# Performance work log

Hardware: AMD Instinct MI355X
Metric: run time of the kernel (lower is better)

The kernel has to match this reference:

```python
import jax, jax.numpy as jnp
import numpy as np

B, C, H, W = 16, 1024, 32, 32  # H*W must equal C (required by matmul(h, fg) in the source)
EPS = 1e-5
NEG_SLOPE = 0.01


def setup_inputs() -> dict:
    key = jax.random.key(0)
    ks = jax.random.split(key, 12)
    s = 1.0 / np.sqrt(C)
    inp = {"x": jax.random.normal(ks[0], (B, C, H, W), jnp.float32)}
    for i, name in enumerate(["f", "g", "h", "c"]):
        inp[f"W{name}"] = jax.random.normal(ks[1 + 2 * i], (C, C), jnp.float32) * s
        inp[f"b{name}"] = jax.random.normal(ks[2 + 2 * i], (C,), jnp.float32) * 0.01
    inp["gamma"] = jnp.ones((C,), jnp.float32)
    inp["beta"] = jnp.zeros((C,), jnp.float32)
    inp["rmean"] = jax.random.normal(ks[9], (C,), jnp.float32) * 0.01
    inp["rvar"] = jax.random.uniform(ks[10], (C,), jnp.float32, 0.5, 1.5)
    return inp


def reference(x, Wf, bf, Wg, bg, Wh, bh, Wc, bc, gamma, beta, rmean, rvar):
    b, c, h_, w_ = x.shape
    n = h_ * w_  # == c by construction
    xf = x.reshape(b, c, n)

    def proj(Wp, bp):  # 1x1 conv == per-pixel channel matmul
        return jnp.einsum('oc,bcn->bon', Wp, xf) + bp[None, :, None]

    f = proj(Wf, bf)              # (B, C, N)
    g = proj(Wg, bg)              # (B, C, N); transposed(1,2) handled in einsum
    hh = proj(Wh, bh)             # (B, C, N)
    scores = jnp.einsum('bcn,bdn->bcd', f, g)        # f @ g^T -> (B, C, C)
    attn = jax.nn.softmax(scores, axis=1)            # softmax over dim=1 (as in source)
    # dropout2d(p=0.5) is identity in eval mode
    hfg = jnp.einsum('bcn,bnd->bcd', hh, attn)       # matmul(h, fg), needs N == C
    hfg = hfg.reshape(b, c, h_, w_)
    y = jnp.einsum('oc,bchw->bohw', Wc, hfg) + bc[None, :, None, None]
    y = jnp.where(y >= 0, y, NEG_SLOPE * y)          # LeakyReLU
    inv = gamma / jnp.sqrt(rvar + EPS)               # BatchNorm (eval mode)
    y = (y - rmean[None, :, None, None]) * inv[None, :, None, None] + beta[None, :, None, None]
    return y + x
```

## Files before the change

kernel.cpp:

```cpp
#include <hip/hip_runtime.h>
#include <cstdint>
#include <cstddef>

using half8  = __attribute__((ext_vector_type(8))) _Float16;
using half4  = __attribute__((ext_vector_type(4))) _Float16;
using float4v = __attribute__((ext_vector_type(4))) float;

#define CD 1024
#define M2 (1024 * 1024)

#define GLD16(gp, lp)                                                          \
    __builtin_amdgcn_global_load_lds(                                          \
        (const __attribute__((address_space(1))) void*)(gp),                   \
        (__attribute__((address_space(3))) void*)(lp), 16, 0, 0)

__global__ void prep_weights(const float* __restrict__ Wf, const float* __restrict__ Wg,
                             const float* __restrict__ Wh, const float* __restrict__ Wc,
                             const float* __restrict__ bf, const float* __restrict__ bg,
                             const float* __restrict__ bh,
                             _Float16* __restrict__ Wfgh, _Float16* __restrict__ WcH,
                             float* __restrict__ bstack) {
    int idx = blockIdx.x * 256 + threadIdx.x;
    if (idx < 3 * M2) {
        const float* s = idx < M2 ? Wf : (idx < 2 * M2 ? Wg : Wh);
        int off = idx & (M2 - 1);
        Wfgh[idx] = (_Float16)s[off];
    } else if (idx < 4 * M2) {
        WcH[idx - 3 * M2] = (_Float16)Wc[idx - 3 * M2];
    } else if (idx < 4 * M2 + 3 * CD) {
        int j = idx - 4 * M2;
        const float* s = j < CD ? bf : (j < 2 * CD ? bg : bh);
        bstack[j] = s[j & (CD - 1)];
    }
}

__global__ void transpose_x(const float* __restrict__ x, _Float16* __restrict__ xT, int b0) {
    __shared__ float tile[32][33];
    int z = blockIdx.z;
    const float* xb = x + (size_t)(b0 + z) * M2;
    _Float16* xTb = xT + (size_t)z * M2;
    int n0 = blockIdx.x * 32, k0 = blockIdx.y * 32;
    int tx = threadIdx.x, ty = threadIdx.y;
#pragma unroll
    for (int i = 0; i < 4; i++)
        tile[ty + i * 8][tx] = xb[(size_t)(k0 + ty + i * 8) * CD + n0 + tx];
    __syncthreads();
#pragma unroll
    for (int i = 0; i < 4; i++)
        xTb[(size_t)(n0 + ty + i * 8) * CD + k0 + tx] = (_Float16)tile[tx][ty + i * 8];
}

__global__ __launch_bounds__(256) void softmax_col(const float* __restrict__ ST,
                                                   _Float16* __restrict__ attnT) {
    int d = blockIdx.x, z = blockIdx.y;
    const float* row = ST + ((size_t)z * CD + d) * CD;
    _Float16* orow = attnT + ((size_t)z * CD + d) * CD;
    int t = threadIdx.x;
    float4v v = *(const float4v*)(row + t * 4);
    float mx = fmaxf(fmaxf(v[0], v[1]), fmaxf(v[2], v[3]));
#pragma unroll
    for (int o = 32; o > 0; o >>= 1) mx = fmaxf(mx, __shfl_xor(mx, o));
    __shared__ float redm[4], reds[4];
    int wave = t >> 6, lane = t & 63;
    if (lane == 0) redm[wave] = mx;
    __syncthreads();
    mx = fmaxf(fmaxf(redm[0], redm[1]), fmaxf(redm[2], redm[3]));
    float e[4];
    float s = 0.f;
#pragma unroll
    for (int i = 0; i < 4; i++) {
        e[i] = __expf(v[i] - mx);
        s += e[i];
    }
#pragma unroll
    for (int o = 32; o > 0; o >>= 1) s += __shfl_xor(s, o);
    if (lane == 0) reds[wave] = s;
    __syncthreads();
    s = reds[0] + reds[1] + reds[2] + reds[3];
    float inv = 1.0f / s;
    half4 ov;
#pragma unroll
    for (int i = 0; i < 4; i++) ov[i] = (_Float16)(e[i] * inv);
    *(half4*)(orow + t * 4) = ov;
}

enum { EP_F16B = 0, EP_F32 = 1, EP_F16 = 2, EP_FIN = 3 };

#define STAGE_A(T, BUF)                                                        \
    GLD16(gA0 + (size_t)(T) * 32, &As[BUF][wv * 16][0]);                       \
    GLD16(gA1 + (size_t)(T) * 32, &As[BUF][128 + wv * 16][0]);
#define STAGE_B(T, BUF)                                                        \
    GLD16(gB0 + (size_t)(T) * 32, &Bs[BUF][wv * 16][0]);                       \
    GLD16(gB1 + (size_t)(T) * 32, &Bs[BUF][128 + wv * 16][0]);

#define MFMA_HALF(M0)                                                          \
    __builtin_amdgcn_s_setprio(1);                                             \
    _Pragma("unroll") for (int m = M0; m < (M0) + 4; m++)                      \
        _Pragma("unroll") for (int n = 0; n < 4; n++)                          \
            acc[m][n] = __builtin_amdgcn_mfma_f32_16x16x32_f16(                \
                a[m], b[n], acc[m][n], 0, 0, 0);                               \
    __builtin_amdgcn_s_setprio(0);

#define PHASE_A(BUF, SA, SAT, SAB)                                             \
    {                                                                          \
        _Pragma("unroll") for (int m = 0; m < 4; m++)                          \
            a[m] = *(const half8*)&As[BUF][wr * 128 + m * 16 + rl][kqa];       \
        _Pragma("unroll") for (int n = 0; n < 4; n++)                          \
            b[n] = *(const half8*)&Bs[BUF][wc * 64 + n * 16 + rl][kqa];        \
        if (SA) { STAGE_A(SAT, SAB) }                                          \
        __builtin_amdgcn_s_barrier();                                          \
        asm volatile("s_waitcnt lgkmcnt(0)" ::: "memory");                     \
        __builtin_amdgcn_sched_barrier(0);                                     \
        MFMA_HALF(0)                                                           \
        __builtin_amdgcn_s_barrier();                                          \
    }

#define PHASE_B(BUF, SB, SBT, SBB, VM, VMS, EBAR)                              \
    {                                                                          \
        _Pragma("unroll") for (int m = 4; m < 8; m++)                          \
            a[m] = *(const half8*)&As[BUF][wr * 128 + m * 16 + rl][kqa];       \
        if (SB) { STAGE_B(SBT, SBB) }                                          \
        __builtin_amdgcn_s_barrier();                                          \
        asm volatile("s_waitcnt lgkmcnt(0)" ::: "memory");                     \
        __builtin_amdgcn_sched_barrier(0);                                     \
        MFMA_HALF(4)                                                           \
        if (VM) {                                                              \
            asm volatile("s_waitcnt " VMS ::: "memory");                       \
            __builtin_amdgcn_sched_barrier(0);                                 \
        }                                                                      \
        if (EBAR) __builtin_amdgcn_s_barrier();                                \
    }

template <int EPI>
__global__ __launch_bounds__(512, 2) void gemm_nt(
    const _Float16* __restrict__ A, int64_t sA, const _Float16* __restrict__ B, int64_t sB,
    void* __restrict__ Cp, int64_t sC, const float* __restrict__ bias,
    const float* __restrict__ bc, const float* __restrict__ gamma,
    const float* __restrict__ beta, const float* __restrict__ rmean,
    const float* __restrict__ rvar, const float* __restrict__ xres) {
    __shared__ __align__(16) _Float16 As[4][256][32];
    __shared__ __align__(16) _Float16 Bs[4][256][32];
    int z = blockIdx.z;
    const _Float16* Ab = A + (size_t)z * sA;
    const _Float16* Bb = B + (size_t)z * sB;
    int row0 = blockIdx.y * 256, col0 = blockIdx.x * 256;
    int tid = threadIdx.x, lane = tid & 63, wv = tid >> 6;
    int wr = wv >> 2, wc = wv & 3;

    const int srow = wv * 16 + (lane >> 2);
    const int scol = ((lane & 3) ^ ((lane >> 3) & 3)) * 8;
    const _Float16* gA0 = Ab + (size_t)(row0 + srow) * 1024 + scol;
    const _Float16* gA1 = gA0 + (size_t)128 * 1024;
    const _Float16* gB0 = Bb + (size_t)(col0 + srow) * 1024 + scol;
    const _Float16* gB1 = gB0 + (size_t)128 * 1024;

    const int rl = lane & 15;
    const int kq = (lane >> 4) * 8;
    const int kqa = kq ^ (((rl >> 1) & 3) << 3);

    float4v acc[8][4] = {};
    half8 a[8], b[4];

    STAGE_A(0, 0) STAGE_B(0, 0) STAGE_A(1, 1) STAGE_B(1, 1)
    STAGE_A(2, 2) STAGE_B(2, 2) STAGE_B(3, 3)
    asm volatile("s_waitcnt vmcnt(10)" ::: "memory");
    __builtin_amdgcn_sched_barrier(0);
    __builtin_amdgcn_s_barrier();

#pragma unroll 1
    for (int tq = 0; tq < 7; ++tq) {
        int t = tq * 4;
        PHASE_A(0, 1, t + 3, 3) PHASE_B(0, 1, t + 4, 0, 1, "vmcnt(10)", 1)
        PHASE_A(1, 1, t + 4, 0) PHASE_B(1, 1, t + 5, 1, 1, "vmcnt(10)", 1)
        PHASE_A(2, 1, t + 5, 1) PHASE_B(2, 1, t + 6, 2, 1, "vmcnt(10)", 1)
        PHASE_A(3, 1, t + 6, 2) PHASE_B(3, 1, t + 7, 3, 1, "vmcnt(10)", 1)
    }
    PHASE_A(0, 1, 31, 3) PHASE_B(0, 0, 0, 0, 1, "vmcnt(8)", 1)
    PHASE_A(1, 0, 0, 0)  PHASE_B(1, 0, 0, 0, 1, "vmcnt(4)", 1)
    PHASE_A(2, 0, 0, 0)  PHASE_B(2, 0, 0, 0, 1, "vmcnt(0)", 1)
    PHASE_A(3, 0, 0, 0)  PHASE_B(3, 0, 0, 0, 0, "", 0)

#pragma unroll
    for (int m = 0; m < 8; m++) {
#pragma unroll
        for (int r = 0; r < 4; r++) {
            int row = row0 + wr * 128 + m * 16 + ((lane >> 4) << 2) + r;
            float add0 = 0.f, mu = 0.f, invs = 1.f, bet = 0.f;
            if constexpr (EPI == EP_F16B) add0 = bias[row];
            if constexpr (EPI == EP_FIN) {
                add0 = bc[row];
                mu = rmean[row];
                invs = gamma[row] * rsqrtf(rvar[row] + 1e-5f);
                bet = beta[row];
            }
#pragma unroll
            for (int n = 0; n < 4; n++) {
                int col = col0 + wc * 64 + n * 16 + (lane & 15);
                float v = acc[m][n][r];
                if constexpr (EPI == EP_F16B) {
                    ((_Float16*)Cp)[(size_t)z * sC + (size_t)row * 1024 + col] = (_Float16)(v + add0);
                } else if constexpr (EPI == EP_F32) {
                    ((float*)Cp)[(size_t)z * sC + (size_t)row * 1024 + col] = v;
                } else if constexpr (EPI == EP_F16) {
                    ((_Float16*)Cp)[(size_t)z * sC + (size_t)row * 1024 + col] = (_Float16)v;
                } else {
                    v += add0;
                    v = v >= 0.f ? v : 0.01f * v;
                    v = (v - mu) * invs + bet;
                    v += xres[(size_t)z * M2 + (size_t)row * 1024 + col];
                    ((float*)Cp)[(size_t)z * sC + (size_t)row * 1024 + col] = v;
                }
            }
        }
    }
}

extern "C" void kernel_launch(void* const* d_in, const int* in_sizes, int n_in,
                              void* d_out, int out_size, void* d_ws, size_t ws_size,
                              hipStream_t stream) {
    const float* x = (const float*)d_in[0];
    const float* Wf = (const float*)d_in[1];
    const float* bf = (const float*)d_in[2];
    const float* Wg = (const float*)d_in[3];
    const float* bg = (const float*)d_in[4];
    const float* Wh = (const float*)d_in[5];
    const float* bh = (const float*)d_in[6];
    const float* Wc = (const float*)d_in[7];
    const float* bc = (const float*)d_in[8];
    const float* gamma = (const float*)d_in[9];
    const float* beta = (const float*)d_in[10];
    const float* rmean = (const float*)d_in[11];
    const float* rvar = (const float*)d_in[12];

    char* p = (char*)d_ws;
    _Float16* Wfgh = (_Float16*)p;
    p += (size_t)3 * M2 * 2;
    _Float16* WcH = (_Float16*)p;
    p += (size_t)M2 * 2;
    float* bstack = (float*)p;
    p += (size_t)3 * CD * 4;
    size_t fixed = (size_t)(p - (char*)d_ws);
    fixed = (fixed + 255) & ~(size_t)255;

    size_t perB = (size_t)2 * M2 + (size_t)6 * M2 + (size_t)4 * M2;
    int nb = 16;
    while (nb > 1 && fixed + (size_t)nb * perB > ws_size) nb >>= 1;

    {
        int total = 4 * M2 + 3 * CD;
        prep_weights<<<dim3((total + 255) / 256), dim3(256), 0, stream>>>(
            Wf, Wg, Wh, Wc, bf, bg, bh, Wfgh, WcH, bstack);
    }

    for (int b0 = 0; b0 < 16; b0 += nb) {
        char* q = (char*)d_ws + fixed;
        _Float16* xT = (_Float16*)q;
        _Float16* FGH = (_Float16*)(q + (size_t)nb * 2 * M2);
        float* ST = (float*)(q + (size_t)nb * 8 * M2);
        _Float16* attnT = xT;
        _Float16* hfgT = (_Float16*)ST;

        transpose_x<<<dim3(32, 32, nb), dim3(32, 8), 0, stream>>>(x, xT, b0);
        gemm_nt<EP_F16B><<<dim3(4, 12, nb), dim3(512), 0, stream>>>(
            Wfgh, 0, xT, M2, FGH, (int64_t)3 * M2, bstack,
            nullptr, nullptr, nullptr, nullptr, nullptr, nullptr);
        gemm_nt<EP_F32><<<dim3(4, 4, nb), dim3(512), 0, stream>>>(
            FGH + M2, (int64_t)3 * M2, FGH, (int64_t)3 * M2, ST, M2,
            nullptr, nullptr, nullptr, nullptr, nullptr, nullptr, nullptr);
        softmax_col<<<dim3(1024, nb), dim3(256), 0, stream>>>(ST, attnT);
        gemm_nt<EP_F16><<<dim3(4, 4, nb), dim3(512), 0, stream>>>(
            attnT, M2, FGH + 2 * M2, (int64_t)3 * M2, hfgT, M2,
            nullptr, nullptr, nullptr, nullptr, nullptr, nullptr, nullptr);
        gemm_nt<EP_FIN><<<dim3(4, 4, nb), dim3(512), 0, stream>>>(
            WcH, 0, hfgT, M2, (float*)d_out + (size_t)b0 * M2, M2,
            nullptr, bc, gamma, beta, rmean, rvar, x + (size_t)b0 * M2);
    }
}
```

Measured before the change: 311.8 us.

## Collapse two-phase half-tile GEMM schedule into one barrier per K-tile

Replaces the split PHASE_A/PHASE_B main loop with a single TILE step per K-tile. Each step waits on global loads, takes one workgroup barrier, reads all A/B fragments from LDS, issues the A and B prefetch together, then runs all 32 MFMAs at raised priority. The prologue now stages three full tiles and the vmcnt thresholds are adjusted to match. This cuts the barriers per tile from four to one, but gives up the finer interleaving of LDS reads and global prefetch with the two MFMA halves.

```diff
diff --git a/kernel.cpp b/kernel.cpp
--- a/kernel.cpp
+++ b/kernel.cpp
@@ -93,42 +93,25 @@
     GLD16(gB0 + (size_t)(T) * 32, &Bs[BUF][wv * 16][0]);                       \
     GLD16(gB1 + (size_t)(T) * 32, &Bs[BUF][128 + wv * 16][0]);
 
-#define MFMA_HALF(M0)                                                          \
-    __builtin_amdgcn_s_setprio(1);                                             \
-    _Pragma("unroll") for (int m = M0; m < (M0) + 4; m++)                      \
-        _Pragma("unroll") for (int n = 0; n < 4; n++)                          \
-            acc[m][n] = __builtin_amdgcn_mfma_f32_16x16x32_f16(                \
-                a[m], b[n], acc[m][n], 0, 0, 0);                               \
-    __builtin_amdgcn_s_setprio(0);
-
-#define PHASE_A(BUF, SA, SAT, SAB)                                             \
+#define TILE(BUF, DOSTAGE, STT, STBUF, VMSTR)                                  \
     {                                                                          \
+        asm volatile("s_waitcnt " VMSTR ::: "memory");                         \
+        __builtin_amdgcn_sched_barrier(0);                                     \
+        __builtin_amdgcn_s_barrier();                                          \
         _Pragma("unroll") for (int m = 0; m < 4; m++)                          \
             a[m] = *(const half8*)&As[BUF][wr * 128 + m * 16 + rl][kqa];       \
         _Pragma("unroll") for (int n = 0; n < 4; n++)                          \
             b[n] = *(const half8*)&Bs[BUF][wc * 64 + n * 16 + rl][kqa];        \
-        if (SA) { STAGE_A(SAT, SAB) }                                          \
-        __builtin_amdgcn_s_barrier();                                          \
-        asm volatile("s_waitcnt lgkmcnt(0)" ::: "memory");                     \
-        __builtin_amdgcn_sched_barrier(0);                                     \
-        MFMA_HALF(0)                                                           \
-        __builtin_amdgcn_s_barrier();                                          \
-    }
-
-#define PHASE_B(BUF, SB, SBT, SBB, VM, VMS, EBAR)                              \
-    {                                                                          \
         _Pragma("unroll") for (int m = 4; m < 8; m++)                          \
             a[m] = *(const half8*)&As[BUF][wr * 128 + m * 16 + rl][kqa];       \
-        if (SB) { STAGE_B(SBT, SBB) }                                          \
-        __builtin_amdgcn_s_barrier();                                          \
-        asm volatile("s_waitcnt lgkmcnt(0)" ::: "memory");                     \
+        if (DOSTAGE) { STAGE_A(STT, STBUF) STAGE_B(STT, STBUF) }               \
         __builtin_amdgcn_sched_barrier(0);                                     \
-        MFMA_HALF(4)                                                           \
-        if (VM) {                                                              \
-            asm volatile("s_waitcnt " VMS ::: "memory");                       \
-            __builtin_amdgcn_sched_barrier(0);                                 \
-        }                                                                      \
-        if (EBAR) __builtin_amdgcn_s_barrier();                                \
+        __builtin_amdgcn_s_setprio(1);                                         \
+        _Pragma("unroll") for (int m = 0; m < 8; m++)                          \
+            _Pragma("unroll") for (int n = 0; n < 4; n++)                      \
+                acc[m][n] = __builtin_amdgcn_mfma_f32_16x16x32_f16(            \
+                    a[m], b[n], acc[m][n], 0, 0, 0);                           \
+        __builtin_amdgcn_s_setprio(0);                                         \
     }
 
 template <int EPI>
@@ -161,24 +144,22 @@
     float4v acc[8][4] = {};
     half8 a[8], b[4];
 
-    STAGE_A(0, 0) STAGE_B(0, 0) STAGE_A(1, 1) STAGE_B(1, 1)
-    STAGE_A(2, 2) STAGE_B(2, 2) STAGE_B(3, 3)
-    asm volatile("s_waitcnt vmcnt(10)" ::: "memory");
-    __builtin_amdgcn_sched_barrier(0);
-    __builtin_amdgcn_s_barrier();
+    STAGE_A(0, 0) STAGE_B(0, 0)
+    STAGE_A(1, 1) STAGE_B(1, 1)
+    STAGE_A(2, 2) STAGE_B(2, 2)
 
 #pragma unroll 1
-    for (int tq = 0; tq < 7; ++tq) {
-        int t = tq * 4;
-        PHASE_A(0, 1, t + 3, 3) PHASE_B(0, 1, t + 4, 0, 1, "vmcnt(10)", 1)
-        PHASE_A(1, 1, t + 4, 0) PHASE_B(1, 1, t + 5, 1, 1, "vmcnt(10)", 1)
-        PHASE_A(2, 1, t + 5, 1) PHASE_B(2, 1, t + 6, 2, 1, "vmcnt(10)", 1)
-        PHASE_A(3, 1, t + 6, 2) PHASE_B(3, 1, t + 7, 3, 1, "vmcnt(10)", 1)
-    }
-    PHASE_A(0, 1, 31, 3) PHASE_B(0, 0, 0, 0, 1, "vmcnt(8)", 1)
-    PHASE_A(1, 0, 0, 0)  PHASE_B(1, 0, 0, 0, 1, "vmcnt(4)", 1)
-    PHASE_A(2, 0, 0, 0)  PHASE_B(2, 0, 0, 0, 1, "vmcnt(0)", 1)
-    PHASE_A(3, 0, 0, 0)  PHASE_B(3, 0, 0, 0, 0, "", 0)
+    for (int g = 0; g < 7; ++g) {
+        int t = g * 4;
+        TILE(0, 1, t + 3, 3, "vmcnt(8)")
+        TILE(1, 1, t + 4, 0, "vmcnt(8)")
+        TILE(2, 1, t + 5, 1, "vmcnt(8)")
+        TILE(3, 1, t + 6, 2, "vmcnt(8)")
+    }
+    TILE(0, 1, 31, 3, "vmcnt(8)")
+    TILE(1, 0, 0, 0, "vmcnt(8)")
+    TILE(2, 0, 0, 0, "vmcnt(4)")
+    TILE(3, 0, 0, 0, "vmcnt(0)")
 
 #pragma unroll
     for (int m = 0; m < 8; m++) {
```

After: 301.3 us. 3.3% less time.
